# Kernel optimization log

Measured on AMD Instinct MI355X. Metric: run time of the kernel, lower is better.

The kernel has to match this reference:

```python
import jax, jax.numpy as jnp
import numpy as np

B, N, K = 4, 20480, 16
LAMDA = 2.0  # config.lfa_param

def _gather(pc, idx):
    # pc: [B, N, D], idx: [B, N, K] -> [B, N, K, D]
    return jax.vmap(lambda p, i: p[i])(pc, idx)

def _cbr(x, W, g, b, act=True):
    # 1x1 conv (no bias) + BN(eval, affine) + optional ReLU; x: [B, C, N, K]
    y = jnp.einsum('oc,bcnk->bonk', W, x)
    y = y * g[None, :, None, None] + b[None, :, None, None]
    return jnp.maximum(y, 0.0) if act else y

def _fdis(feat, f_nb):
    # feat: [B, C, N], f_nb: [B, C, N, K] -> exp(-mean_c |diff|): [B, 1, N, K]
    return jnp.exp(-jnp.mean(jnp.abs(feat[..., None] - f_nb), axis=1, keepdims=True))

def _pool(f_set, f_dis, g_dis, fcW, mW, mg, mb):
    # Dualdis_Att_Pool: softmax attention over neighbor dim K
    concat = jnp.concatenate([g_dis, f_dis * LAMDA, f_set], axis=1)
    att = jax.nn.softmax(jnp.einsum('oc,bcnk->bonk', fcW, concat), axis=3)
    f_lc = jnp.sum(f_set * att, axis=-1, keepdims=True)
    return _cbr(f_lc, mW, mg, mb)

def _forward(feature, xyz, m1_W, m1_g, m1_b, lm1_W, lm1_g, lm1_b, lm2_W, lm2_g, lm2_b, p1fc_W, p1m_W, p1m_g, p1m_b, p2fc_W, p2m_W, p2m_g, p2m_b, m2_W, m2_g, m2_b, sc_W, sc_g, sc_b, m3_W, m3_g, m3_b, m4_W, m4_g, m4_b, neigh_idx):
    f_pc = _cbr(feature, m1_W, m1_g, m1_b)               # [B,16,N,1]
    # --- local polar representation ---
    nb = _gather(xyz, neigh_idx)                         # [B,N,K,3]
    xyz_t = xyz[:, :, None, :]
    rel = xyz_t - nb
    r_alpha = jnp.arctan2(rel[..., 1], rel[..., 0])[..., None]
    r_beta = jnp.arctan2(rel[..., 2], jnp.sqrt(rel[..., 0]**2 + rel[..., 1]**2))[..., None]
    r_dis = jnp.sqrt(jnp.sum(rel * rel, axis=-1, keepdims=True))
    rel_info = jnp.concatenate([r_dis, jnp.broadcast_to(xyz_t, nb.shape), nb], axis=-1)
    g_dis = jnp.exp(-r_dis)                              # [B,N,K,1]
    local_vol = jnp.max(r_dis[..., 0], axis=-1) ** 3     # [B,N]
    dirv = xyz - jnp.mean(nb, axis=2)                    # [B,N,3]
    d_alpha = jnp.arctan2(dirv[..., 1], dirv[..., 0])[:, :, None, None]
    d_beta = jnp.arctan2(dirv[..., 2], jnp.sqrt(dirv[..., 0]**2 + dirv[..., 1]**2))[:, :, None, None]
    angle = jnp.concatenate([r_alpha - d_alpha, r_beta - d_beta], axis=-1)
    local_rep = jnp.concatenate([angle, rel_info], axis=-1)  # [B,N,K,9]
    g_vol = jnp.sqrt(jnp.sum(xyz * xyz, axis=-1)) ** 3
    lg_ratio = (local_vol / g_vol)[..., None]            # [B,N,1]
    g_dis = jnp.transpose(g_dis, (0, 3, 1, 2))           # [B,1,N,K]
    lrep = _cbr(jnp.transpose(local_rep, (0, 3, 1, 2)), lm1_W, lm1_g, lm1_b)  # [B,16,N,K]
    # --- dual-distance attentive pooling 1 ---
    feat0 = f_pc[..., 0]
    f_nb = jnp.transpose(_gather(jnp.transpose(feat0, (0, 2, 1)), neigh_idx), (0, 3, 1, 2))
    f_cat = jnp.concatenate([f_nb, lrep], axis=1)        # [B,32,N,K]
    f_lc = _pool(f_cat, _fdis(feat0, f_nb), g_dis, p1fc_W, p1m_W, p1m_g, p1m_b)  # [B,16,N,1]
    # --- dual-distance attentive pooling 2 ---
    lrep2 = _cbr(lrep, lm2_W, lm2_g, lm2_b)
    feat1 = f_lc[..., 0]
    f_nb2 = jnp.transpose(_gather(jnp.transpose(feat1, (0, 2, 1)), neigh_idx), (0, 3, 1, 2))
    f_cat2 = jnp.concatenate([f_nb2, lrep2], axis=1)     # [B,32,N,K]
    f_lc2 = _pool(f_cat2, _fdis(feat1, f_nb2), g_dis, p2fc_W, p2m_W, p2m_g, p2m_b)  # [B,32,N,1]
    # --- residual head ---
    out_lc = _cbr(f_lc2, m2_W, m2_g, m2_b, act=False)
    sc = _cbr(feature, sc_W, sc_g, sc_b, act=False)
    f_gc_in = jnp.transpose(jnp.concatenate([xyz, lg_ratio], axis=-1), (0, 2, 1))[..., None]
    f_gc = _cbr(f_gc_in, m3_W, m3_g, m3_b, act=False)
    return _cbr(jnp.concatenate([out_lc + sc, f_gc], axis=1), m4_W, m4_g, m4_b)  # [B,64,N,1]

def setup_inputs():
    key = jax.random.key(0)
    ks = iter(jax.random.split(key, 48))
    def rn(shape, s=1.0):
        return jax.random.normal(next(ks), shape, jnp.float32) * s
    inp = {"feature": rn((B, 16, N, 1)), "xyz": rn((B, N, 3))}
    def wgb(name, co, ci):
        inp[name + "_W"] = rn((co, ci), 0.1)
        inp[name + "_g"] = jax.random.uniform(next(ks), (co,), jnp.float32, 0.5, 1.5)
        inp[name + "_b"] = jnp.zeros((co,), jnp.float32)
    wgb("m1", 16, 16); wgb("lm1", 16, 9); wgb("lm2", 16, 16)
    inp["p1fc_W"] = rn((32, 34), 0.1); wgb("p1m", 16, 32)
    inp["p2fc_W"] = rn((32, 34), 0.1); wgb("p2m", 32, 32)
    wgb("m2", 64, 32); wgb("sc", 64, 16); wgb("m3", 64, 4); wgb("m4", 64, 128)
    inp["neigh_idx"] = jax.random.randint(next(ks), (B, N, K), 0, N)
    return inp

def reference(feature, xyz, m1_W, m1_g, m1_b, lm1_W, lm1_g, lm1_b, lm2_W, lm2_g, lm2_b, p1fc_W, p1m_W, p1m_g, p1m_b, p2fc_W, p2m_W, p2m_g, p2m_b, m2_W, m2_g, m2_b, sc_W, sc_g, sc_b, m3_W, m3_g, m3_b, m4_W, m4_g, m4_b, neigh_idx):
    return _forward(feature, xyz, m1_W, m1_g, m1_b, lm1_W, lm1_g, lm1_b, lm2_W, lm2_g, lm2_b, p1fc_W, p1m_W, p1m_g, p1m_b, p2fc_W, p2m_W, p2m_g, p2m_b, m2_W, m2_g, m2_b, sc_W, sc_g, sc_b, m3_W, m3_g, m3_b, m4_W, m4_g, m4_b, neigh_idx)
```

## Files before the change

kernel.cpp:

```cpp
#include <hip/hip_runtime.h>

#define NN 20480
#define NPTS 81920
#define MS 36
#define RSH 40
#define PTSH 640
#define MIDOFF 2560
#define LOG2E 1.4426950408889634f

#define P1MWT 0
#define P2MWT 512
#define MAWT  1536
#define MXWT  3584
#define MVWT  4608
#define C0WT  4864
#define BFB   4928
#define WTOT  6976

#define WL_P2M 0
#define WL_MA  1024
#define WL_MX  3072
#define WL_MV  4096
#define WL_C0  4352
#define WOFF   4416
#define SLAB   1280
#define LGRO   (WOFF + 4*SLAB)
#define SMTOT2 9600

typedef _Float16 half8 __attribute__((ext_vector_type(8)));
typedef float f32x4 __attribute__((ext_vector_type(4)));

__device__ __forceinline__ float redsum16(float v){
    v += __shfl_xor(v, 1); v += __shfl_xor(v, 2);
    v += __shfl_xor(v, 4); v += __shfl_xor(v, 8);
    return v;
}
__device__ __forceinline__ float redmax16(float v){
    v = fmaxf(v, __shfl_xor(v, 1)); v = fmaxf(v, __shfl_xor(v, 2));
    v = fmaxf(v, __shfl_xor(v, 4)); v = fmaxf(v, __shfl_xor(v, 8));
    return v;
}
__device__ __forceinline__ void wsync(){
    __builtin_amdgcn_wave_barrier();
    __threadfence_block();
    __builtin_amdgcn_wave_barrier();
}
__device__ __forceinline__ float frcp(float x){ return __builtin_amdgcn_rcpf(x); }

__device__ __forceinline__ unsigned int ph(float lo, float hi){
    union { _Float16 h[2]; unsigned int u; } cv;
    cv.h[0] = (_Float16)lo; cv.h[1] = (_Float16)hi;
    return cv.u;
}
__device__ __forceinline__ float2 unph(unsigned int u){
    union { unsigned int u; _Float16 h[2]; } cv; cv.u = u;
    return make_float2((float)cv.h[0], (float)cv.h[1]);
}
__device__ __forceinline__ float h2f(short s){
    union { short s; _Float16 h; } cv; cv.s = s;
    return (float)cv.h;
}

__device__ __forceinline__ float fatan2(float y, float x){
    float ax = fabsf(x), ay = fabsf(y);
    float mx = fmaxf(ax, ay), mn = fminf(ax, ay);
    float z = mn * frcp(mx);
    z = (mx == 0.f) ? 0.f : z;
    float z2 = z * z;
    float a = fmaf(0.05265332f, z2, -0.11643287f);
    a = fmaf(a, z2, 0.19354346f);
    a = fmaf(a, z2, -0.33262347f);
    a = fmaf(a, z2, 0.99997726f);
    a = a * z;
    a = (ay > ax) ? (1.5707963268f - a) : a;
    a = (x < 0.f) ? (3.1415926536f - a) : a;
    return (y < 0.f) ? -a : a;
}

__device__ __forceinline__ int swiz(int bid){
    int x = bid & 7, s = bid >> 3;
    return ((x >> 1) * 2560) + ((x & 1) * 1280) + s;
}
__device__ __forceinline__ int swizC(int bid){
    int x = bid & 7, s = bid >> 3;
    return x * 160 + s;
}

__global__ void k_fill4(float4* out, float val, int n4){
    int i = blockIdx.x * blockDim.x + threadIdx.x;
    int stride = gridDim.x * blockDim.x;
    float4 v = make_float4(val, val, val, val);
    for (; i < n4; i += stride) out[i] = v;
}

__global__ void k_prep(
    const float* __restrict__ p1fc, const float* __restrict__ p2fc,
    const float* __restrict__ p1mW, const float* __restrict__ p2mW,
    const float* __restrict__ m2W,  const float* __restrict__ scW,
    const float* __restrict__ m3W,  const float* __restrict__ m4W,
    const float* __restrict__ m2g,  const float* __restrict__ m2b,
    const float* __restrict__ scg,  const float* __restrict__ scb,
    const float* __restrict__ m3g,  const float* __restrict__ m3b,
    float* __restrict__ wb)
{
    int bid = blockIdx.x;
    if (bid == 0){
        for (int e = threadIdx.x; e < 512; e += 256)
            wb[P1MWT + e] = p1mW[e];
    } else if (bid == 1){
        for (int e = threadIdx.x; e < 1024; e += 256){
            int c = e >> 5, r = e & 31;
            int k = r >> 1, h = r & 1;
            wb[P2MWT + e] = p2mW[(k + 16*h)*32 + c];
        }
    } else if (bid == 2){
        for (int e = threadIdx.x; e < 2048; e += 256){
            int c = e >> 6, r = e & 63;
            int o = (r >> 2) + 16*(r & 3);
            float acc = 0.f;
            for (int h = 0; h < 64; h++)
                acc = fmaf(m4W[o*128 + h] * m2g[h], m2W[h*32 + c], acc);
            wb[MAWT + e] = acc;
        }
    } else if (bid == 3){
        for (int e = threadIdx.x; e < 1024; e += 256){
            int c = e >> 6, r = e & 63;
            int o = (r >> 2) + 16*(r & 3);
            float acc = 0.f;
            for (int h = 0; h < 64; h++)
                acc = fmaf(m4W[o*128 + h] * scg[h], scW[h*16 + c], acc);
            wb[MXWT + e] = acc;
        }
    } else if (bid == 4){
        int e = threadIdx.x;
        if (e < 256){
            int c = e >> 6, r = e & 63;
            int o = (r >> 2) + 16*(r & 3);
            float acc = 0.f;
            for (int h = 0; h < 64; h++)
                acc = fmaf(m4W[o*128 + 64 + h] * m3g[h], m3W[h*4 + c], acc);
            wb[MVWT + e] = acc;
        }
        if (e < 64){
            int o = (e >> 2) + 16*(e & 3);
            float acc = 0.f;
            for (int h = 0; h < 64; h++){
                acc = fmaf(m4W[o*128 + h], m2b[h] + scb[h], acc);
                acc = fmaf(m4W[o*128 + 64 + h], m3b[h], acc);
            }
            wb[C0WT + e] = acc;
        }
    } else if (bid == 6 || bid == 7){
        const float* src = (bid == 6) ? p1fc : p2fc;
        short* dst = (short*)(wb + BFB) + (bid - 6) * 2048;
        for (int e = threadIdx.x; e < 2048; e += 256){
            int j = e & 7, l = (e >> 3) & 63, tq = (e >> 9) & 3;
            int q = tq & 1, t = tq >> 1;
            int kk = ((l >> 4) << 3) + j;
            int c = q*32 + kk;
            int o = (l & 15) + 16*t;
            float v = (c < 34) ? src[o*34 + c] * LOG2E : 0.f;
            union { _Float16 h; short s; } cv; cv.h = (_Float16)v;
            dst[e] = cv.s;
        }
    }
}

__global__ __launch_bounds__(256) void k_feat0(
    const float* __restrict__ featp,
    const float* __restrict__ m1W,
    const float* __restrict__ m1g,
    const float* __restrict__ m1b,
    float* __restrict__ feat0)
{
    int p = blockIdx.x * 256 + threadIdx.x;
    if (p >= NPTS) return;
    int b = p / NN;
    int n = p - b * NN;
    float x[16];
    #pragma unroll
    for (int c = 0; c < 16; c++) x[c] = featp[(b*16 + c)*NN + n];
    float o[16];
    for (int oo = 0; oo < 16; oo++){
        float acc = 0.f;
        #pragma unroll
        for (int c = 0; c < 16; c++) acc = fmaf(m1W[oo*16 + c], x[c], acc);
        o[oo] = fmaxf(fmaf(m1g[oo], acc, m1b[oo]), 0.f);
    }
    float4* dst = (float4*)(feat0 + (size_t)p * 16);
    #pragma unroll
    for (int i = 0; i < 4; i++)
        dst[i] = make_float4(o[4*i], o[4*i+1], o[4*i+2], o[4*i+3]);
}

__device__ __forceinline__ float poolT(f32x4 a, const short* base, int c, int g){
    const short* xc = base + c;
    float x0 = h2f(xc[(g*4 + 0)*RSH]), x1 = h2f(xc[(g*4 + 1)*RSH]);
    float x2 = h2f(xc[(g*4 + 2)*RSH]), x3 = h2f(xc[(g*4 + 3)*RSH]);
    float m = fmaxf(fmaxf(a[0], a[1]), fmaxf(a[2], a[3]));
    m = fmaxf(m, __shfl_xor(m, 16)); m = fmaxf(m, __shfl_xor(m, 32));
    float e0 = exp2f(a[0] - m), e1 = exp2f(a[1] - m);
    float e2 = exp2f(a[2] - m), e3 = exp2f(a[3] - m);
    float s = (e0 + e1) + (e2 + e3);
    float num = fmaf(e3, x3, fmaf(e2, x2, fmaf(e1, x1, e0*x0)));
    s   += __shfl_xor(s, 16);   s   += __shfl_xor(s, 32);
    num += __shfl_xor(num, 16); num += __shfl_xor(num, 32);
    return num * frcp(s);
}

__device__ __forceinline__ void phaseB_mfma(
    const short* xs, const short* bfS, float* smMid, int tid)
{
    const half8* bf = (const half8*)bfS;
    const int l = tid & 63, wv = tid >> 6;
    const int o = l & 15, g = l >> 4;
    half8 B00 = bf[l], B01 = bf[64 + l], B10 = bf[128 + l], B11 = bf[192 + l];
    #pragma unroll 2
    for (int pp = 0; pp < 4; pp++){
        const int pt = wv*4 + pp;
        const short* base = xs + pt*PTSH;
        const short* rowp = base + (l & 15)*RSH;
        half8 A0 = *(const half8*)(rowp + g*8);
        unsigned int d = *(const unsigned int*)(rowp + 32);
        union { unsigned int u[4]; half8 v; } a1u;
        a1u.u[0] = (g == 0) ? d : 0u;
        a1u.u[1] = 0u; a1u.u[2] = 0u; a1u.u[3] = 0u;
        half8 A1 = a1u.v;
        f32x4 z = {0.f, 0.f, 0.f, 0.f};
        f32x4 a0 = __builtin_amdgcn_mfma_f32_16x16x32_f16(A0, B00, z, 0, 0, 0);
        a0       = __builtin_amdgcn_mfma_f32_16x16x32_f16(A1, B01, a0, 0, 0, 0);
        f32x4 a1 = __builtin_amdgcn_mfma_f32_16x16x32_f16(A0, B10, z, 0, 0, 0);
        a1       = __builtin_amdgcn_mfma_f32_16x16x32_f16(A1, B11, a1, 0, 0, 0);
        float mid0 = poolT(a0, base, 2 + o,      g);
        float mid1 = poolT(a1, base, 2 + o + 16, g);
        if (g == 0){
            smMid[pt*MS + o]      = mid0;
            smMid[pt*MS + o + 16] = mid1;
        }
    }
}

__global__ __launch_bounds__(128, 2) void k_stage1(
    const float* __restrict__ xyzp,
    const int* __restrict__ nidx,
    const float* __restrict__ feat0,
    const float* __restrict__ lm1W,
    const float* __restrict__ lm1g,
    const float* __restrict__ lm1b,
    const float* __restrict__ wb,
    const float* __restrict__ p1mg,
    const float* __restrict__ p1mb,
    float* __restrict__ feat1)
{
    __shared__ float sm[2848];
    short* xs = (short*)sm;
    const int k  = threadIdx.x & 15;
    const int pt = threadIdx.x >> 4;
    const int p  = (swiz(blockIdx.x) << 3) + pt;
    const int b  = p / NN;

    {
        const int ii = nidx[(p << 4) + k];
        const int q  = b * NN + ii;
        const float4* an = (const float4*)(feat0 + (size_t)q * 16);
        const float4* as = (const float4*)(feat0 + (size_t)p * 16);
        const float sx = xyzp[p*3 + 0];
        const float sy = xyzp[p*3 + 1];
        const float sz = xyzp[p*3 + 2];
        const float nx = xyzp[q*3 + 0];
        const float ny = xyzp[q*3 + 1];
        const float nz = xyzp[q*3 + 2];

        float4 A0 = an[0], A1 = an[1], A2 = an[2], A3 = an[3];
        float sd = 0.f;
        {
            float4 S0 = as[0], S1 = as[1], S2 = as[2], S3 = as[3];
            sd += fabsf(S0.x-A0.x) + fabsf(S0.y-A0.y) + fabsf(S0.z-A0.z) + fabsf(S0.w-A0.w);
            sd += fabsf(S1.x-A1.x) + fabsf(S1.y-A1.y) + fabsf(S1.z-A1.z) + fabsf(S1.w-A1.w);
            sd += fabsf(S2.x-A2.x) + fabsf(S2.y-A2.y) + fabsf(S2.z-A2.z) + fabsf(S2.w-A2.w);
            sd += fabsf(S3.x-A3.x) + fabsf(S3.y-A3.y) + fabsf(S3.z-A3.z) + fabsf(S3.w-A3.w);
        }
        float fdis2 = 2.f * __expf(-sd * 0.0625f);

        float rx = sx - nx, ry = sy - ny, rz = sz - nz;
        float r2 = rx*rx + ry*ry;
        float rdis = sqrtf(r2 + rz*rz);
        float ralpha = fatan2(ry, rx);
        float rbeta  = fatan2(rz, sqrtf(r2));
        float gdis = __expf(-rdis);

        float mx = redsum16(nx) * 0.0625f;
        float my = redsum16(ny) * 0.0625f;
        float mz = redsum16(nz) * 0.0625f;
        float dx = sx - mx, dy = sy - my, dz = sz - mz;
        float dalpha = fatan2(dy, dx);
        float dbeta  = fatan2(dz, sqrtf(dx*dx + dy*dy));

        float rep[9] = { ralpha - dalpha, rbeta - dbeta, rdis, sx, sy, sz, nx, ny, nz };
        float lrep[16];
        #pragma unroll
        for (int o = 0; o < 16; o++){
            float acc = 0.f;
            #pragma unroll
            for (int c = 0; c < 9; c++) acc = fmaf(lm1W[o*9 + c], rep[c], acc);
            lrep[o] = fmaxf(fmaf(lm1g[o], acc, lm1b[o]), 0.f);
        }

        uint4* rp = (uint4*)(xs + pt*PTSH + k*RSH);
        uint4 U;
        U.x = ph(gdis, fdis2); U.y = ph(A0.x, A0.y);
        U.z = ph(A0.z, A0.w);  U.w = ph(A1.x, A1.y);
        rp[0] = U;
        U.x = ph(A1.z, A1.w);  U.y = ph(A2.x, A2.y);
        U.z = ph(A2.z, A2.w);  U.w = ph(A3.x, A3.y);
        rp[1] = U;
        U.x = ph(A3.z, A3.w);      U.y = ph(lrep[0], lrep[1]);
        U.z = ph(lrep[2], lrep[3]); U.w = ph(lrep[4], lrep[5]);
        rp[2] = U;
        U.x = ph(lrep[6], lrep[7]);   U.y = ph(lrep[8], lrep[9]);
        U.z = ph(lrep[10], lrep[11]); U.w = ph(lrep[12], lrep[13]);
        rp[3] = U;
        U.x = ph(lrep[14], lrep[15]); U.y = 0u; U.z = 0u; U.w = 0u;
        rp[4] = U;
    }
    wsync();

    phaseB_mfma(xs, (const short*)(wb + BFB), sm + MIDOFF, threadIdx.x);
    wsync();

    {
        float mid[32];
        const float4* mp = (const float4*)(sm + MIDOFF + pt*MS);
        #pragma unroll
        for (int i = 0; i < 8; i++){
            float4 t = mp[i];
            mid[4*i]=t.x; mid[4*i+1]=t.y; mid[4*i+2]=t.z; mid[4*i+3]=t.w;
        }
        const float4* wp = (const float4*)(wb + P1MWT) + (k << 3);
        float acc = 0.f;
        #pragma unroll
        for (int i = 0; i < 8; i++){
            float4 wv = wp[i];
            acc = fmaf(wv.x, mid[4*i],   acc);
            acc = fmaf(wv.y, mid[4*i+1], acc);
            acc = fmaf(wv.z, mid[4*i+2], acc);
            acc = fmaf(wv.w, mid[4*i+3], acc);
        }
        feat1[(size_t)(p << 4) + k] = fmaxf(fmaf(p1mg[k], acc, p1mb[k]), 0.f);
    }
}

__global__ __launch_bounds__(128, 2) void k_s2ab(
    const float* __restrict__ xyzp,
    const int* __restrict__ nidx,
    const float* __restrict__ feat1,
    const float* __restrict__ lm1W,
    const float* __restrict__ lm1g,
    const float* __restrict__ lm1b,
    const float* __restrict__ lm2W,
    const float* __restrict__ lm2g,
    const float* __restrict__ lm2b,
    const float* __restrict__ wb,
    float* __restrict__ outp)
{
    __shared__ float sm[2848];
    short* xs = (short*)sm;
    const int k    = threadIdx.x & 15;
    const int pt   = threadIdx.x >> 4;
    const int pblk = swiz(blockIdx.x);
    const int p    = (pblk << 3) + pt;
    const int b    = p / NN;
    const int n    = p - b * NN;
    float lgrv;

    {
        const int ii = nidx[(p << 4) + k];
        const int q  = b * NN + ii;
        const float4* an = (const float4*)(feat1 + (size_t)q * 16);
        const float4* as = (const float4*)(feat1 + (size_t)p * 16);
        const float sx = xyzp[p*3 + 0];
        const float sy = xyzp[p*3 + 1];
        const float sz = xyzp[p*3 + 2];
        const float nx = xyzp[q*3 + 0];
        const float ny = xyzp[q*3 + 1];
        const float nz = xyzp[q*3 + 2];

        float4 A0 = an[0], A1 = an[1], A2 = an[2], A3 = an[3];
        float sd = 0.f;
        {
            float4 S0 = as[0], S1 = as[1], S2 = as[2], S3 = as[3];
            sd += fabsf(S0.x-A0.x) + fabsf(S0.y-A0.y) + fabsf(S0.z-A0.z) + fabsf(S0.w-A0.w);
            sd += fabsf(S1.x-A1.x) + fabsf(S1.y-A1.y) + fabsf(S1.z-A1.z) + fabsf(S1.w-A1.w);
            sd += fabsf(S2.x-A2.x) + fabsf(S2.y-A2.y) + fabsf(S2.z-A2.z) + fabsf(S2.w-A2.w);
            sd += fabsf(S3.x-A3.x) + fabsf(S3.y-A3.y) + fabsf(S3.z-A3.z) + fabsf(S3.w-A3.w);
        }
        float fdis2 = 2.f * __expf(-sd * 0.0625f);

        float rx = sx - nx, ry = sy - ny, rz = sz - nz;
        float r2 = rx*rx + ry*ry;
        float rdis = sqrtf(r2 + rz*rz);
        float ralpha = fatan2(ry, rx);
        float rbeta  = fatan2(rz, sqrtf(r2));
        float gdis = __expf(-rdis);

        float mx = redsum16(nx) * 0.0625f;
        float my = redsum16(ny) * 0.0625f;
        float mz = redsum16(nz) * 0.0625f;
        float dx = sx - mx, dy = sy - my, dz = sz - mz;
        float dalpha = fatan2(dy, dx);
        float dbeta  = fatan2(dz, sqrtf(dx*dx + dy*dy));

        float mxd = redmax16(rdis);
        float nr  = sqrtf(sx*sx + sy*sy + sz*sz);
        lgrv = (mxd*mxd*mxd) * frcp(nr*nr*nr);

        float rep[9] = { ralpha - dalpha, rbeta - dbeta, rdis, sx, sy, sz, nx, ny, nz };
        float lrep[16];
        #pragma unroll
        for (int o = 0; o < 16; o++){
            float acc = 0.f;
            #pragma unroll
            for (int c = 0; c < 9; c++) acc = fmaf(lm1W[o*9 + c], rep[c], acc);
            lrep[o] = fmaxf(fmaf(lm1g[o], acc, lm1b[o]), 0.f);
        }
        float lrep2[16];
        #pragma unroll
        for (int o = 0; o < 16; o++){
            float acc = 0.f;
            #pragma unroll
            for (int c = 0; c < 16; c++) acc = fmaf(lm2W[o*16 + c], lrep[c], acc);
            lrep2[o] = fmaxf(fmaf(lm2g[o], acc, lm2b[o]), 0.f);
        }

        uint4* rp = (uint4*)(xs + pt*PTSH + k*RSH);
        uint4 U;
        U.x = ph(gdis, fdis2); U.y = ph(A0.x, A0.y);
        U.z = ph(A0.z, A0.w);  U.w = ph(A1.x, A1.y);
        rp[0] = U;
        U.x = ph(A1.z, A1.w);  U.y = ph(A2.x, A2.y);
        U.z = ph(A2.z, A2.w);  U.w = ph(A3.x, A3.y);
        rp[1] = U;
        U.x = ph(A3.z, A3.w);        U.y = ph(lrep2[0], lrep2[1]);
        U.z = ph(lrep2[2], lrep2[3]); U.w = ph(lrep2[4], lrep2[5]);
        rp[2] = U;
        U.x = ph(lrep2[6], lrep2[7]);   U.y = ph(lrep2[8], lrep2[9]);
        U.z = ph(lrep2[10], lrep2[11]); U.w = ph(lrep2[12], lrep2[13]);
        rp[3] = U;
        U.x = ph(lrep2[14], lrep2[15]); U.y = 0u; U.z = 0u; U.w = 0u;
        rp[4] = U;
    }
    wsync();

    phaseB_mfma(xs, (const short*)(wb + BFB) + 2048, sm + MIDOFF, threadIdx.x);
    wsync();

    {
        float m0 = sm[MIDOFF + pt*MS + 2*k];
        float m1 = sm[MIDOFF + pt*MS + 2*k + 1];
        unsigned int u = ph(m0, m1);
        ((unsigned int*)outp)[(size_t)(b*64 + k)*NN + n] = u;
        if (k == 0) outp[(size_t)(b*64 + 16)*NN + n] = lgrv;
    }
}

__global__ __launch_bounds__(256, 2) void k_s2c(
    const float* __restrict__ featp,
    const float* __restrict__ xyzp,
    const float* __restrict__ wb,
    const float* __restrict__ p2mg,
    const float* __restrict__ p2mb,
    const float* __restrict__ m4g,
    const float* __restrict__ m4b,
    float* __restrict__ outp)
{
    __shared__ float sm[SMTOT2];
    const int tid = threadIdx.x;
    const int k   = tid & 15;
    const int g   = (tid >> 4) & 3;
    const int w   = tid >> 6;
    const int pblk = swizC(blockIdx.x);
    const int p0  = pblk << 6;
    const int b   = p0 / NN;
    const int n0  = p0 - b * NN;
    const int ptg = g*4;
    const int nT  = n0 + w*16 + ptg;
    float* slab = sm + WOFF + w*SLAB;

    for (int e = tid; e < 4416; e += 256) sm[e] = wb[512 + e];
    {
        uint4 um = *(const uint4*)((const unsigned int*)outp +
                                   (size_t)(b*64 + k)*NN + nT);
        float2 f;
        f = unph(um.x);
        slab[(ptg+0)*36 + 2*k] = f.x; slab[(ptg+0)*36 + 2*k+1] = f.y;
        f = unph(um.y);
        slab[(ptg+1)*36 + 2*k] = f.x; slab[(ptg+1)*36 + 2*k+1] = f.y;
        f = unph(um.z);
        slab[(ptg+2)*36 + 2*k] = f.x; slab[(ptg+2)*36 + 2*k+1] = f.y;
        f = unph(um.w);
        slab[(ptg+3)*36 + 2*k] = f.x; slab[(ptg+3)*36 + 2*k+1] = f.y;
        if (k == 0){
            float4 lv = *(const float4*)(outp + (size_t)(b*64 + 16)*NN + nT);
            sm[LGRO + w*16 + ptg + 0] = lv.x; sm[LGRO + w*16 + ptg + 1] = lv.y;
            sm[LGRO + w*16 + ptg + 2] = lv.z; sm[LGRO + w*16 + ptg + 3] = lv.w;
        }
    }
    __syncthreads();

    {
        const float2* wp = (const float2*)(sm + WL_P2M);
        float aA[4] = {0.f,0.f,0.f,0.f}, aB[4] = {0.f,0.f,0.f,0.f};
        #pragma unroll 2
        for (int cq = 0; cq < 8; cq++){
            f32x4 mv[4];
            #pragma unroll
            for (int i = 0; i < 4; i++)
                mv[i] = *(const f32x4*)(slab + (ptg+i)*36 + cq*4);
            #pragma unroll
            for (int cc = 0; cc < 4; cc++){
                float2 wv = wp[(cq*4+cc)*16 + k];
                #pragma unroll
                for (int i = 0; i < 4; i++){
                    aA[i] = fmaf(wv.x, mv[i][cc], aA[i]);
                    aB[i] = fmaf(wv.y, mv[i][cc], aB[i]);
                }
            }
        }
        float gA = p2mg[k], bA = p2mb[k], gB = p2mg[k+16], bB = p2mb[k+16];
        #pragma unroll
        for (int i = 0; i < 4; i++){
            slab[576 + (ptg+i)*36 + k]      = fmaxf(fmaf(gA, aA[i], bA), 0.f);
            slab[576 + (ptg+i)*36 + k + 16] = fmaxf(fmaf(gB, aB[i], bB), 0.f);
        }
    }
    wsync();

    float o4[4][4];
    {
        f32x4 c0v = *(const f32x4*)(sm + WL_C0 + 4*k);
        #pragma unroll
        for (int j = 0; j < 4; j++)
            #pragma unroll
            for (int i = 0; i < 4; i++) o4[j][i] = c0v[j];

        const f32x4* wa = (const f32x4*)(sm + WL_MA);
        #pragma unroll 2
        for (int cq = 0; cq < 8; cq++){
            f32x4 av[4];
            #pragma unroll
            for (int i = 0; i < 4; i++)
                av[i] = *(const f32x4*)(slab + 576 + (ptg+i)*36 + cq*4);
            #pragma unroll
            for (int cc = 0; cc < 4; cc++){
                f32x4 wv = wa[(cq*4+cc)*16 + k];
                #pragma unroll
                for (int i = 0; i < 4; i++){
                    #pragma unroll
                    for (int j = 0; j < 4; j++)
                        o4[j][i] = fmaf(wv[j], av[i][cc], o4[j][i]);
                }
            }
        }
        const f32x4* wx = (const f32x4*)(sm + WL_MX);
        #pragma unroll 4
        for (int c = 0; c < 16; c++){
            f32x4 wv = wx[c*16 + k];
            f32x4 xv = *(const f32x4*)(featp + (size_t)(b*16 + c)*NN + nT);
            #pragma unroll
            for (int i = 0; i < 4; i++){
                #pragma unroll
                for (int j = 0; j < 4; j++)
                    o4[j][i] = fmaf(wv[j], xv[i], o4[j][i]);
            }
        }
        const f32x4* wvv = (const f32x4*)(sm + WL_MV);
        #pragma unroll
        for (int c = 0; c < 3; c++){
            f32x4 wv = wvv[c*16 + k];
            #pragma unroll
            for (int i = 0; i < 4; i++){
                float vc = xyzp[(size_t)(p0 + w*16 + ptg + i)*3 + c];
                #pragma unroll
                for (int j = 0; j < 4; j++)
                    o4[j][i] = fmaf(wv[j], vc, o4[j][i]);
            }
        }
        {
            f32x4 wv = wvv[3*16 + k];
            #pragma unroll
            for (int i = 0; i < 4; i++){
                float vc = sm[LGRO + w*16 + ptg + i];
                #pragma unroll
                for (int j = 0; j < 4; j++)
                    o4[j][i] = fmaf(wv[j], vc, o4[j][i]);
            }
        }
    }
    wsync();

    {
        float* stg = slab;
        #pragma unroll
        for (int j = 0; j < 4; j++){
            int oo = k + 16*j;
            float gv = m4g[oo], bv = m4b[oo];
            #pragma unroll
            for (int i = 0; i < 4; i++)
                stg[oo*20 + ptg + i] = fmaxf(fmaf(gv, o4[j][i], bv), 0.f);
        }
        wsync();
        const int l = tid & 63;
        float* dst = outp + (size_t)(b*64 + l)*NN + n0 + w*16;
        #pragma unroll
        for (int q = 0; q < 4; q++){
            f32x4 v = *(const f32x4*)(stg + l*20 + q*4);
            *(f32x4*)(dst + q*4) = v;
        }
    }
}

extern "C" void kernel_launch(void* const* d_in, const int* in_sizes, int n_in,
                              void* d_out, int out_size, void* d_ws, size_t ws_size,
                              hipStream_t stream) {
    float* outp = (float*)d_out;

    float fillv = 1.0f;
    bool ok = true;
    if (n_in != 32) { fillv = 5.0f; ok = false; }
    else if (in_sizes[0] != 1310720 || in_sizes[1] != 245760 ||
             in_sizes[31] != 1310720) { fillv = 7.0f; ok = false; }
    else if (out_size != 5242880) { fillv = 9.0f; ok = false; }
    else if (ws_size < ((size_t)NPTS * 16 + WTOT) * sizeof(float)) { fillv = 11.0f; ok = false; }

    if (!ok){
        k_fill4<<<1024, 256, 0, stream>>>((float4*)outp, fillv, out_size/4);
        return;
    }

    const float* featp = (const float*)d_in[0];
    const float* xyzp  = (const float*)d_in[1];
    const int*   nidx  = (const int*)d_in[31];

    float* feat0 = (float*)d_out;
    float* feat1 = (float*)d_ws;
    float* wb    = (float*)d_ws + (size_t)NPTS * 16;

    #define W(i) ((const float*)d_in[2 + (i)])
    k_prep<<<8, 256, 0, stream>>>(W(9), W(13), W(10), W(14), W(17), W(20),
                                  W(23), W(26),
                                  W(18), W(19), W(21), W(22), W(24), W(25),
                                  wb);
    k_feat0<<<NPTS/256, 256, 0, stream>>>(featp, W(0), W(1), W(2), feat0);
    k_stage1<<<NPTS/8, 128, 0, stream>>>(xyzp, nidx, feat0,
        W(3), W(4), W(5), wb, W(11), W(12), feat1);
    k_s2ab<<<NPTS/8, 128, 0, stream>>>(xyzp, nidx, feat1,
        W(3), W(4), W(5),
        W(6), W(7), W(8),
        wb, outp);
    k_s2c<<<NPTS/64, 256, 0, stream>>>(featp, xyzp, wb,
        W(15), W(16),
        W(27), W(28),
        outp);
    #undef W
}
```

Before: 253.7 us.

## Store intermediates in fp16, split lm1 linearly, reuse geometry across stages

Merges weight prep and the m1 conv into one launch, stores feat0/feat1 as fp16, and splits the lm1 conv into per-point center and neighbor partial sums precomputed once. Stage 1 writes the angles, distance and volume ratio to scratch rows of the output, so stage 2 reads them instead of redoing the gathers, atan2 and reductions. L1 feature distances are computed with packed half arithmetic. This cuts gather bandwidth and redundant math, at the cost of extra fp16 rounding error and more scratch traffic.

```diff
diff --git a/kernel.cpp b/kernel.cpp
--- a/kernel.cpp
+++ b/kernel.cpp
@@ -6,7 +6,13 @@
 #define RSH 40
 #define PTSH 640
 #define MIDOFF 2560
+#define HSOFF 2848
 #define LOG2E 1.4426950408889634f
+
+#define HSROW 17
+#define PAROW 25
+#define PBROW 41
+#define LGROW 57
 
 #define P1MWT 0
 #define P2MWT 512
@@ -15,20 +21,13 @@
 #define MVWT  4608
 #define C0WT  4864
 #define BFB   4928
-#define WTOT  6976
-
-#define WL_P2M 0
-#define WL_MA  1024
-#define WL_MX  3072
-#define WL_MV  4096
-#define WL_C0  4352
-#define WOFF   4416
-#define SLAB   1280
-#define LGRO   (WOFF + 4*SLAB)
-#define SMTOT2 9600
+#define LM1AW 6976
+#define WTOT  7040
 
 typedef _Float16 half8 __attribute__((ext_vector_type(8)));
+typedef _Float16 h2t  __attribute__((ext_vector_type(2)));
 typedef float f32x4 __attribute__((ext_vector_type(4)));
+union HU { unsigned int u; h2t h; };
 
 __device__ __forceinline__ float redsum16(float v){
     v += __shfl_xor(v, 1); v += __shfl_xor(v, 2);
@@ -56,9 +55,15 @@
     union { unsigned int u; _Float16 h[2]; } cv; cv.u = u;
     return make_float2((float)cv.h[0], (float)cv.h[1]);
 }
-__device__ __forceinline__ float h2f(short s){
-    union { short s; _Float16 h; } cv; cv.s = s;
-    return (float)cv.h;
+
+__device__ __forceinline__ float sd16(uint4 a0, uint4 a1, uint4 b0, uint4 b1){
+    HU acc; acc.u = 0u;
+    #define SDT(A,B) { HU x,y,d; x.u=(A); y.u=(B); d.h = x.h - y.h; \
+                       d.u &= 0x7FFF7FFFu; acc.h = acc.h + d.h; }
+    SDT(a0.x,b0.x) SDT(a0.y,b0.y) SDT(a0.z,b0.z) SDT(a0.w,b0.w)
+    SDT(a1.x,b1.x) SDT(a1.y,b1.y) SDT(a1.z,b1.z) SDT(a1.w,b1.w)
+    #undef SDT
+    return (float)acc.h[0] + (float)acc.h[1];
 }
 
 __device__ __forceinline__ float fatan2(float y, float x){
@@ -93,7 +98,12 @@
     for (; i < n4; i += stride) out[i] = v;
 }
 
-__global__ void k_prep(
+__global__ __launch_bounds__(256) void k_pre(
+    const float* __restrict__ featp, const float* __restrict__ xyzp,
+    const float* __restrict__ m1W,  const float* __restrict__ m1g,
+    const float* __restrict__ m1b,
+    const float* __restrict__ lm1W, const float* __restrict__ lm1g,
+    const float* __restrict__ lm1b,
     const float* __restrict__ p1fc, const float* __restrict__ p2fc,
     const float* __restrict__ p1mW, const float* __restrict__ p2mW,
     const float* __restrict__ m2W,  const float* __restrict__ scW,
@@ -101,102 +111,126 @@
     const float* __restrict__ m2g,  const float* __restrict__ m2b,
     const float* __restrict__ scg,  const float* __restrict__ scb,
     const float* __restrict__ m3g,  const float* __restrict__ m3b,
-    float* __restrict__ wb)
+    float* __restrict__ wb, float* __restrict__ wsF,
+    float* __restrict__ outp)
 {
     int bid = blockIdx.x;
-    if (bid == 0){
-        for (int e = threadIdx.x; e < 512; e += 256)
-            wb[P1MWT + e] = p1mW[e];
-    } else if (bid == 1){
-        for (int e = threadIdx.x; e < 1024; e += 256){
-            int c = e >> 5, r = e & 31;
-            int k = r >> 1, h = r & 1;
-            wb[P2MWT + e] = p2mW[(k + 16*h)*32 + c];
-        }
-    } else if (bid == 2){
-        for (int e = threadIdx.x; e < 2048; e += 256){
-            int c = e >> 6, r = e & 63;
-            int o = (r >> 2) + 16*(r & 3);
-            float acc = 0.f;
-            for (int h = 0; h < 64; h++)
-                acc = fmaf(m4W[o*128 + h] * m2g[h], m2W[h*32 + c], acc);
-            wb[MAWT + e] = acc;
-        }
-    } else if (bid == 3){
-        for (int e = threadIdx.x; e < 1024; e += 256){
-            int c = e >> 6, r = e & 63;
-            int o = (r >> 2) + 16*(r & 3);
-            float acc = 0.f;
-            for (int h = 0; h < 64; h++)
-                acc = fmaf(m4W[o*128 + h] * scg[h], scW[h*16 + c], acc);
-            wb[MXWT + e] = acc;
-        }
-    } else if (bid == 4){
-        int e = threadIdx.x;
-        if (e < 256){
-            int c = e >> 6, r = e & 63;
-            int o = (r >> 2) + 16*(r & 3);
-            float acc = 0.f;
-            for (int h = 0; h < 64; h++)
-                acc = fmaf(m4W[o*128 + 64 + h] * m3g[h], m3W[h*4 + c], acc);
-            wb[MVWT + e] = acc;
-        }
-        if (e < 64){
-            int o = (e >> 2) + 16*(e & 3);
-            float acc = 0.f;
-            for (int h = 0; h < 64; h++){
-                acc = fmaf(m4W[o*128 + h], m2b[h] + scb[h], acc);
-                acc = fmaf(m4W[o*128 + 64 + h], m3b[h], acc);
-            }
-            wb[C0WT + e] = acc;
-        }
-    } else if (bid == 6 || bid == 7){
-        const float* src = (bid == 6) ? p1fc : p2fc;
-        short* dst = (short*)(wb + BFB) + (bid - 6) * 2048;
-        for (int e = threadIdx.x; e < 2048; e += 256){
-            int j = e & 7, l = (e >> 3) & 63, tq = (e >> 9) & 3;
-            int q = tq & 1, t = tq >> 1;
-            int kk = ((l >> 4) << 3) + j;
-            int c = q*32 + kk;
-            int o = (l & 15) + 16*t;
-            float v = (c < 34) ? src[o*34 + c] * LOG2E : 0.f;
-            union { _Float16 h; short s; } cv; cv.h = (_Float16)v;
-            dst[e] = cv.s;
-        }
-    }
-}
-
-__global__ __launch_bounds__(256) void k_feat0(
-    const float* __restrict__ featp,
-    const float* __restrict__ m1W,
-    const float* __restrict__ m1g,
-    const float* __restrict__ m1b,
-    float* __restrict__ feat0)
-{
-    int p = blockIdx.x * 256 + threadIdx.x;
-    if (p >= NPTS) return;
+    if (bid < 8){
+        if (bid == 0){
+            for (int e = threadIdx.x; e < 512; e += 256)
+                wb[P1MWT + e] = p1mW[e];
+        } else if (bid == 1){
+            for (int e = threadIdx.x; e < 1024; e += 256){
+                int c = e >> 5, r = e & 31;
+                int k = r >> 1, h = r & 1;
+                wb[P2MWT + e] = p2mW[(k + 16*h)*32 + c];
+            }
+        } else if (bid == 2){
+            for (int e = threadIdx.x; e < 2048; e += 256){
+                int c = e >> 6, r = e & 63;
+                int o = (r >> 2) + 16*(r & 3);
+                float acc = 0.f;
+                for (int h = 0; h < 64; h++)
+                    acc = fmaf(m4W[o*128 + h] * m2g[h], m2W[h*32 + c], acc);
+                wb[MAWT + e] = acc;
+            }
+        } else if (bid == 3){
+            for (int e = threadIdx.x; e < 1024; e += 256){
+                int c = e >> 6, r = e & 63;
+                int o = (r >> 2) + 16*(r & 3);
+                float acc = 0.f;
+                for (int h = 0; h < 64; h++)
+                    acc = fmaf(m4W[o*128 + h] * scg[h], scW[h*16 + c], acc);
+                wb[MXWT + e] = acc;
+            }
+        } else if (bid == 4){
+            int e = threadIdx.x;
+            if (e < 256){
+                int c = e >> 6, r = e & 63;
+                int o = (r >> 2) + 16*(r & 3);
+                float acc = 0.f;
+                for (int h = 0; h < 64; h++)
+                    acc = fmaf(m4W[o*128 + 64 + h] * m3g[h], m3W[h*4 + c], acc);
+                wb[MVWT + e] = acc;
+            }
+            if (e < 64){
+                int o = (e >> 2) + 16*(e & 3);
+                float acc = 0.f;
+                for (int h = 0; h < 64; h++){
+                    acc = fmaf(m4W[o*128 + h], m2b[h] + scb[h], acc);
+                    acc = fmaf(m4W[o*128 + 64 + h], m3b[h], acc);
+                }
+                wb[C0WT + e] = acc;
+            }
+        } else if (bid == 5){
+            int e = threadIdx.x;
+            if (e < 48){
+                int c = e >> 4, o = e & 15;
+                wb[LM1AW + e] = lm1g[o] * lm1W[o*9 + c];
+            }
+        } else {
+            const float* src = (bid == 6) ? p1fc : p2fc;
+            short* dst = (short*)(wb + BFB) + (bid - 6) * 2048;
+            for (int e = threadIdx.x; e < 2048; e += 256){
+                int j = e & 7, l = (e >> 3) & 63, tq = (e >> 9) & 3;
+                int q = tq & 1, t = tq >> 1;
+                int kk = ((l >> 4) << 3) + j;
+                int c = q*32 + kk;
+                int o = (l & 15) + 16*t;
+                float v = (c < 34) ? src[o*34 + c] * LOG2E : 0.f;
+                union { _Float16 h; short s; } cv; cv.h = (_Float16)v;
+                dst[e] = cv.s;
+            }
+        }
+        return;
+    }
+    int p = (bid - 8) * 256 + threadIdx.x;
     int b = p / NN;
     int n = p - b * NN;
     float x[16];
     #pragma unroll
     for (int c = 0; c < 16; c++) x[c] = featp[(b*16 + c)*NN + n];
-    float o[16];
-    for (int oo = 0; oo < 16; oo++){
-        float acc = 0.f;
-        #pragma unroll
-        for (int c = 0; c < 16; c++) acc = fmaf(m1W[oo*16 + c], x[c], acc);
-        o[oo] = fmaxf(fmaf(m1g[oo], acc, m1b[oo]), 0.f);
-    }
-    float4* dst = (float4*)(feat0 + (size_t)p * 16);
-    #pragma unroll
-    for (int i = 0; i < 4; i++)
-        dst[i] = make_float4(o[4*i], o[4*i+1], o[4*i+2], o[4*i+3]);
+    unsigned int dw[8];
+    for (int oo = 0; oo < 8; oo++){
+        float v0 = 0.f, v1 = 0.f;
+        #pragma unroll
+        for (int c = 0; c < 16; c++){
+            v0 = fmaf(m1W[(2*oo)*16 + c],   x[c], v0);
+            v1 = fmaf(m1W[(2*oo+1)*16 + c], x[c], v1);
+        }
+        v0 = fmaxf(fmaf(m1g[2*oo],   v0, m1b[2*oo]),   0.f);
+        v1 = fmaxf(fmaf(m1g[2*oo+1], v1, m1b[2*oo+1]), 0.f);
+        dw[oo] = ph(v0, v1);
+    }
+    uint4* f0 = (uint4*)(outp + (size_t)b*64*NN + (size_t)n*8);
+    f0[0] = make_uint4(dw[0], dw[1], dw[2], dw[3]);
+    f0[1] = make_uint4(dw[4], dw[5], dw[6], dw[7]);
+
+    float sx = xyzp[p*3 + 0], sy = xyzp[p*3 + 1], sz = xyzp[p*3 + 2];
+    unsigned int* outu = (unsigned int*)outp;
+    unsigned short* hnT = (unsigned short*)wsF + (size_t)NPTS*16;
+    unsigned int hw[8];
+    for (int d = 0; d < 8; d++){
+        float h0, h1, g0, g1;
+        int o0 = 2*d, o1 = 2*d+1;
+        h0 = lm1g[o0]*(lm1W[o0*9+3]*sx + lm1W[o0*9+4]*sy + lm1W[o0*9+5]*sz) + lm1b[o0];
+        h1 = lm1g[o1]*(lm1W[o1*9+3]*sx + lm1W[o1*9+4]*sy + lm1W[o1*9+5]*sz) + lm1b[o1];
+        g0 = lm1g[o0]*(lm1W[o0*9+6]*sx + lm1W[o0*9+7]*sy + lm1W[o0*9+8]*sz);
+        g1 = lm1g[o1]*(lm1W[o1*9+6]*sx + lm1W[o1*9+7]*sy + lm1W[o1*9+8]*sz);
+        outu[((size_t)b*64 + HSROW + d)*NN + n] = ph(h0, h1);
+        hw[d] = ph(g0, g1);
+    }
+    uint4* hq = (uint4*)(hnT + (size_t)p*16);
+    hq[0] = make_uint4(hw[0], hw[1], hw[2], hw[3]);
+    hq[1] = make_uint4(hw[4], hw[5], hw[6], hw[7]);
 }
 
 __device__ __forceinline__ float poolT(f32x4 a, const short* base, int c, int g){
     const short* xc = base + c;
-    float x0 = h2f(xc[(g*4 + 0)*RSH]), x1 = h2f(xc[(g*4 + 1)*RSH]);
-    float x2 = h2f(xc[(g*4 + 2)*RSH]), x3 = h2f(xc[(g*4 + 3)*RSH]);
+    union { short s; _Float16 h; } c0, c1, c2, c3;
+    c0.s = xc[(g*4 + 0)*RSH]; c1.s = xc[(g*4 + 1)*RSH];
+    c2.s = xc[(g*4 + 2)*RSH]; c3.s = xc[(g*4 + 3)*RSH];
+    float x0 = (float)c0.h, x1 = (float)c1.h, x2 = (float)c2.h, x3 = (float)c3.h;
     float m = fmaxf(fmaxf(a[0], a[1]), fmaxf(a[2], a[3]));
     m = fmaxf(m, __shfl_xor(m, 16)); m = fmaxf(m, __shfl_xor(m, 32));
     float e0 = exp2f(a[0] - m), e1 = exp2f(a[1] - m);
@@ -240,30 +274,61 @@
     }
 }
 
+__device__ __forceinline__ void lrep16(
+    const float* __restrict__ la, float da, float db, float rd,
+    const float* hsS, uint4 H0, uint4 H1, unsigned int* lw)
+{
+    unsigned int hn[8] = {H0.x, H0.y, H0.z, H0.w, H1.x, H1.y, H1.z, H1.w};
+    #pragma unroll
+    for (int d = 0; d < 8; d++){
+        HU a, b, s;
+        a.u = __float_as_uint(hsS[d]);
+        b.u = hn[d];
+        s.h = a.h + b.h;
+        int o0 = 2*d, o1 = 2*d+1;
+        float v0 = fmaf(la[o0], da, fmaf(la[16+o0], db, la[32+o0]*rd));
+        float v1 = fmaf(la[o1], da, fmaf(la[16+o1], db, la[32+o1]*rd));
+        v0 = fmaxf(v0 + (float)s.h[0], 0.f);
+        v1 = fmaxf(v1 + (float)s.h[1], 0.f);
+        lw[d] = ph(v0, v1);
+    }
+}
+
 __global__ __launch_bounds__(128, 2) void k_stage1(
     const float* __restrict__ xyzp,
     const int* __restrict__ nidx,
-    const float* __restrict__ feat0,
-    const float* __restrict__ lm1W,
-    const float* __restrict__ lm1g,
-    const float* __restrict__ lm1b,
     const float* __restrict__ wb,
     const float* __restrict__ p1mg,
     const float* __restrict__ p1mb,
-    float* __restrict__ feat1)
+    float* __restrict__ wsF,
+    float* __restrict__ outp)
 {
-    __shared__ float sm[2848];
+    __shared__ float sm[2912];
     short* xs = (short*)sm;
     const int k  = threadIdx.x & 15;
     const int pt = threadIdx.x >> 4;
-    const int p  = (swiz(blockIdx.x) << 3) + pt;
+    const int lane = threadIdx.x & 63, wv = threadIdx.x >> 6;
+    const int pblk = swiz(blockIdx.x);
+    const int p  = (pblk << 3) + pt;
     const int b  = p / NN;
+    const int n  = p - b * NN;
+    const int nb = (pblk << 3) - b * NN;
+    unsigned short* hnT = (unsigned short*)wsF + (size_t)NPTS*16;
+
+    if (lane < 32){
+        int lpt = wv*4 + (lane >> 3), d = lane & 7;
+        sm[HSOFF + wv*32 + lane] =
+            outp[((size_t)b*64 + HSROW + d)*NN + nb + lpt];
+    }
+    wsync();
 
     {
         const int ii = nidx[(p << 4) + k];
         const int q  = b * NN + ii;
-        const float4* an = (const float4*)(feat0 + (size_t)q * 16);
-        const float4* as = (const float4*)(feat0 + (size_t)p * 16);
+        const uint4* aq = (const uint4*)(outp + (size_t)b*64*NN + (size_t)ii*8);
+        const uint4* ap = (const uint4*)(outp + (size_t)b*64*NN + (size_t)n*8);
+        uint4 A0 = aq[0], A1 = aq[1];
+        uint4 S0 = ap[0], S1 = ap[1];
         const float sx = xyzp[p*3 + 0];
         const float sy = xyzp[p*3 + 1];
         const float sz = xyzp[p*3 + 2];
@@ -271,15 +336,7 @@
         const float ny = xyzp[q*3 + 1];
         const float nz = xyzp[q*3 + 2];
 
-        float4 A0 = an[0], A1 = an[1], A2 = an[2], A3 = an[3];
-        float sd = 0.f;
-        {
-            float4 S0 = as[0], S1 = as[1], S2 = as[2], S3 = as[3];
-            sd += fabsf(S0.x-A0.x) + fabsf(S0.y-A0.y) + fabsf(S0.z-A0.z) + fabsf(S0.w-A0.w);
-            sd += fabsf(S1.x-A1.x) + fabsf(S1.y-A1.y) + fabsf(S1.z-A1.z) + fabsf(S1.w-A1.w);
-            sd += fabsf(S2.x-A2.x) + fabsf(S2.y-A2.y) + fabsf(S2.z-A2.z) + fabsf(S2.w-A2.w);
-            sd += fabsf(S3.x-A3.x) + fabsf(S3.y-A3.y) + fabsf(S3.z-A3.z) + fabsf(S3.w-A3.w);
-        }
+        float sd = sd16(A0, A1, S0, S1);
         float fdis2 = 2.f * __expf(-sd * 0.0625f);
 
         float rx = sx - nx, ry = sy - ny, rz = sz - nz;
@@ -295,33 +352,29 @@
         float dx = sx - mx, dy = sy - my, dz = sz - mz;
         float dalpha = fatan2(dy, dx);
         float dbeta  = fatan2(dz, sqrtf(dx*dx + dy*dy));
-
-        float rep[9] = { ralpha - dalpha, rbeta - dbeta, rdis, sx, sy, sz, nx, ny, nz };
-        float lrep[16];
-        #pragma unroll
-        for (int o = 0; o < 16; o++){
-            float acc = 0.f;
-            #pragma unroll
-            for (int c = 0; c < 9; c++) acc = fmaf(lm1W[o*9 + c], rep[c], acc);
-            lrep[o] = fmaxf(fmaf(lm1g[o], acc, lm1b[o]), 0.f);
-        }
+        float da = ralpha - dalpha, db = rbeta - dbeta;
+
+        float mxd = redmax16(rdis);
+        float nr  = sqrtf(sx*sx + sy*sy + sz*sz);
+
+        unsigned int* outu = (unsigned int*)outp;
+        outu[((size_t)b*64 + PAROW + k)*NN + n] = ph(da, db);
+        outu[((size_t)b*64 + PBROW + k)*NN + n] = ph(rdis, gdis);
+        if (k == 0)
+            outp[((size_t)b*64 + LGROW)*NN + n] = (mxd*mxd*mxd) * frcp(nr*nr*nr);
+
+        const uint4* hq = (const uint4*)(hnT + (size_t)q*16);
+        uint4 H0 = hq[0], H1 = hq[1];
+        unsigned int lw[8];
+        lrep16(wb + LM1AW, da, db, rdis,
+               sm + HSOFF + wv*32 + (pt & 3)*8, H0, H1, lw);
 
         uint4* rp = (uint4*)(xs + pt*PTSH + k*RSH);
-        uint4 U;
-        U.x = ph(gdis, fdis2); U.y = ph(A0.x, A0.y);
-        U.z = ph(A0.z, A0.w);  U.w = ph(A1.x, A1.y);
-        rp[0] = U;
-        U.x = ph(A1.z, A1.w);  U.y = ph(A2.x, A2.y);
-        U.z = ph(A2.z, A2.w);  U.w = ph(A3.x, A3.y);
-        rp[1] = U;
-        U.x = ph(A3.z, A3.w);      U.y = ph(lrep[0], lrep[1]);
-        U.z = ph(lrep[2], lrep[3]); U.w = ph(lrep[4], lrep[5]);
-        rp[2] = U;
-        U.x = ph(lrep[6], lrep[7]);   U.y = ph(lrep[8], lrep[9]);
-        U.z = ph(lrep[10], lrep[11]); U.w = ph(lrep[12], lrep[13]);
-        rp[3] = U;
-        U.x = ph(lrep[14], lrep[15]); U.y = 0u; U.z = 0u; U.w = 0u;
-        rp[4] = U;
+        rp[0] = make_uint4(ph(gdis, fdis2), A0.x, A0.y, A0.z);
+        rp[1] = make_uint4(A0.w, A1.x, A1.y, A1.z);
+        rp[2] = make_uint4(A1.w, lw[0], lw[1], lw[2]);
+        rp[3] = make_uint4(lw[3], lw[4], lw[5], lw[6]);
+        rp[4] = make_uint4(lw[7], 0u, 0u, 0u);
     }
     wsync();
 
@@ -340,114 +393,96 @@
         float acc = 0.f;
         #pragma unroll
         for (int i = 0; i < 8; i++){
-            float4 wv = wp[i];
-            acc = fmaf(wv.x, mid[4*i],   acc);
-            acc = fmaf(wv.y, mid[4*i+1], acc);
-            acc = fmaf(wv.z, mid[4*i+2], acc);
-            acc = fmaf(wv.w, mid[4*i+3], acc);
-        }
-        feat1[(size_t)(p << 4) + k] = fmaxf(fmaf(p1mg[k], acc, p1mb[k]), 0.f);
+            float4 wv4 = wp[i];
+            acc = fmaf(wv4.x, mid[4*i],   acc);
+            acc = fmaf(wv4.y, mid[4*i+1], acc);
+            acc = fmaf(wv4.z, mid[4*i+2], acc);
+            acc = fmaf(wv4.w, mid[4*i+3], acc);
+        }
+        float v = fmaxf(fmaf(p1mg[k], acc, p1mb[k]), 0.f);
+        union { _Float16 h; unsigned short s; } cv; cv.h = (_Float16)v;
+        ((unsigned short*)wsF)[(size_t)(p << 4) + k] = cv.s;
     }
 }
 
 __global__ __launch_bounds__(128, 2) void k_s2ab(
-    const float* __restrict__ xyzp,
     const int* __restrict__ nidx,
-    const float* __restrict__ feat1,
-    const float* __restrict__ lm1W,
-    const float* __restrict__ lm1g,
-    const float* __restrict__ lm1b,
     const float* __restrict__ lm2W,
     const float* __restrict__ lm2g,
     const float* __restrict__ lm2b,
     const float* __restrict__ wb,
+    const float* __restrict__ wsF,
     float* __restrict__ outp)
 {
-    __shared__ float sm[2848];
+    __shared__ float sm[2912];
     short* xs = (short*)sm;
     const int k    = threadIdx.x & 15;
     const int pt   = threadIdx.x >> 4;
+    const int lane = threadIdx.x & 63, wv = threadIdx.x >> 6;
     const int pblk = swiz(blockIdx.x);
     const int p    = (pblk << 3) + pt;
     const int b    = p / NN;
     const int n    = p - b * NN;
-    float lgrv;
+    const int nb   = (pblk << 3) - b * NN;
+    const unsigned short* feat1h = (const unsigned short*)wsF;
+    const unsigned short* hnT = (const unsigned short*)wsF + (size_t)NPTS*16;
+
+    if (lane < 32){
+        int lpt = wv*4 + (lane >> 3), d = lane & 7;
+        sm[HSOFF + wv*32 + lane] =
+            outp[((size_t)b*64 + HSROW + d)*NN + nb + lpt];
+    }
+    wsync();
 
     {
         const int ii = nidx[(p << 4) + k];
         const int q  = b * NN + ii;
-        const float4* an = (const float4*)(feat1 + (size_t)q * 16);
-        const float4* as = (const float4*)(feat1 + (size_t)p * 16);
-        const float sx = xyzp[p*3 + 0];
-        const float sy = xyzp[p*3 + 1];
-        const float sz = xyzp[p*3 + 2];
-        const float nx = xyzp[q*3 + 0];
-        const float ny = xyzp[q*3 + 1];
-        const float nz = xyzp[q*3 + 2];
-
-        float4 A0 = an[0], A1 = an[1], A2 = an[2], A3 = an[3];
-        float sd = 0.f;
-        {
-            float4 S0 = as[0], S1 = as[1], S2 = as[2], S3 = as[3];
-            sd += fabsf(S0.x-A0.x) + fabsf(S0.y-A0.y) + fabsf(S0.z-A0.z) + fabsf(S0.w-A0.w);
-            sd += fabsf(S1.x-A1.x) + fabsf(S1.y-A1.y) + fabsf(S1.z-A1.z) + fabsf(S1.w-A1.w);
-            sd += fabsf(S2.x-A2.x) + fabsf(S2.y-A2.y) + fabsf(S2.z-A2.z) + fabsf(S2.w-A2.w);
-            sd += fabsf(S3.x-A3.x) + fabsf(S3.y-A3.y) + fabsf(S3.z-A3.z) + fabsf(S3.w-A3.w);
-        }
+        const unsigned int* outu = (const unsigned int*)outp;
+        unsigned int pa = outu[((size_t)b*64 + PAROW + k)*NN + n];
+        unsigned int pb = outu[((size_t)b*64 + PBROW + k)*NN + n];
+        float2 dab = unph(pa);
+        HU pbu; pbu.u = pb;
+        float rd = (float)pbu.h[0];
+
+        const uint4* aq = (const uint4*)(feat1h + (size_t)q*16);
+        const uint4* ap = (const uint4*)(feat1h + (size_t)p*16);
+        uint4 A0 = aq[0], A1 = aq[1];
+        uint4 S0 = ap[0], S1 = ap[1];
+        float sd = sd16(A0, A1, S0, S1);
         float fdis2 = 2.f * __expf(-sd * 0.0625f);
 
-        float rx = sx - nx, ry = sy - ny, rz = sz - nz;
-        float r2 = rx*rx + ry*ry;
-        float rdis = sqrtf(r2 + rz*rz);
-        float ralpha = fatan2(ry, rx);
-        float rbeta  = fatan2(rz, sqrtf(r2));
-        float gdis = __expf(-rdis);
-
-        float mx = redsum16(nx) * 0.0625f;
-        float my = redsum16(ny) * 0.0625f;
-        float mz = redsum16(nz) * 0.0625f;
-        float dx = sx - mx, dy = sy - my, dz = sz - mz;
-        float dalpha = fatan2(dy, dx);
-        float dbeta  = fatan2(dz, sqrtf(dx*dx + dy*dy));
-
-        float mxd = redmax16(rdis);
-        float nr  = sqrtf(sx*sx + sy*sy + sz*sz);
-        lgrv = (mxd*mxd*mxd) * frcp(nr*nr*nr);
-
-        float rep[9] = { ralpha - dalpha, rbeta - dbeta, rdis, sx, sy, sz, nx, ny, nz };
-        float lrep[16];
-        #pragma unroll
-        for (int o = 0; o < 16; o++){
-            float acc = 0.f;
-            #pragma unroll
-            for (int c = 0; c < 9; c++) acc = fmaf(lm1W[o*9 + c], rep[c], acc);
-            lrep[o] = fmaxf(fmaf(lm1g[o], acc, lm1b[o]), 0.f);
-        }
-        float lrep2[16];
-        #pragma unroll
-        for (int o = 0; o < 16; o++){
-            float acc = 0.f;
-            #pragma unroll
-            for (int c = 0; c < 16; c++) acc = fmaf(lm2W[o*16 + c], lrep[c], acc);
-            lrep2[o] = fmaxf(fmaf(lm2g[o], acc, lm2b[o]), 0.f);
-        }
-
+        const uint4* hq = (const uint4*)(hnT + (size_t)q*16);
+        uint4 H0 = hq[0], H1 = hq[1];
+        unsigned int lw[8];
+        lrep16(wb + LM1AW, dab.x, dab.y, rd,
+               sm + HSOFF + wv*32 + (pt & 3)*8, H0, H1, lw);
+
+        float lr[16];
+        #pragma unroll
+        for (int d = 0; d < 8; d++){
+            float2 f = unph(lw[d]);
+            lr[2*d] = f.x; lr[2*d+1] = f.y;
+        }
+        unsigned int l2[8];
+        for (int oo = 0; oo < 8; oo++){
+            float v0 = 0.f, v1 = 0.f;
+            #pragma unroll
+            for (int c = 0; c < 16; c++){
+                v0 = fmaf(lm2W[(2*oo)*16 + c],   lr[c], v0);
+                v1 = fmaf(lm2W[(2*oo+1)*16 + c], lr[c], v1);
+            }
+            v0 = fmaxf(fmaf(lm2g[2*oo],   v0, lm2b[2*oo]),   0.f);
+            v1 = fmaxf(fmaf(lm2g[2*oo+1], v1, lm2b[2*oo+1]), 0.f);
+            l2[oo] = ph(v0, v1);
+        }
+
+        HU g0; g0.h[0] = pbu.h[1]; g0.h[1] = (_Float16)fdis2;
         uint4* rp = (uint4*)(xs + pt*PTSH + k*RSH);
-        uint4 U;
-        U.x = ph(gdis, fdis2); U.y = ph(A0.x, A0.y);
-        U.z = ph(A0.z, A0.w);  U.w = ph(A1.x, A1.y);
-        rp[0] = U;
-        U.x = ph(A1.z, A1.w);  U.y = ph(A2.x, A2.y);
-        U.z = ph(A2.z, A2.w);  U.w = ph(A3.x, A3.y);
-        rp[1] = U;
-        U.x = ph(A3.z, A3.w);        U.y = ph(lrep2[0], lrep2[1]);
-        U.z = ph(lrep2[2], lrep2[3]); U.w = ph(lrep2[4], lrep2[5]);
-        rp[2] = U;
-        U.x = ph(lrep2[6], lrep2[7]);   U.y = ph(lrep2[8], lrep2[9]);
-        U.z = ph(lrep2[10], lrep2[11]); U.w = ph(lrep2[12], lrep2[13]);
-        rp[3] = U;
-        U.x = ph(lrep2[14], lrep2[15]); U.y = 0u; U.z = 0u; U.w = 0u;
-        rp[4] = U;
+        rp[0] = make_uint4(g0.u, A0.x, A0.y, A0.z);
+        rp[1] = make_uint4(A0.w, A1.x, A1.y, A1.z);
+        rp[2] = make_uint4(A1.w, l2[0], l2[1], l2[2]);
+        rp[3] = make_uint4(l2[3], l2[4], l2[5], l2[6]);
+        rp[4] = make_uint4(l2[7], 0u, 0u, 0u);
     }
     wsync();
 
@@ -457,11 +492,19 @@
     {
         float m0 = sm[MIDOFF + pt*MS + 2*k];
         float m1 = sm[MIDOFF + pt*MS + 2*k + 1];
-        unsigned int u = ph(m0, m1);
-        ((unsigned int*)outp)[(size_t)(b*64 + k)*NN + n] = u;
-        if (k == 0) outp[(size_t)(b*64 + 16)*NN + n] = lgrv;
-    }
-}
+        ((unsigned int*)outp)[(size_t)(b*64 + k)*NN + n] = ph(m0, m1);
+    }
+}
+
+#define WL_P2M 0
+#define WL_MA  1024
+#define WL_MX  3072
+#define WL_MV  4096
+#define WL_C0  4352
+#define WOFF   4416
+#define SLAB   1280
+#define LGRO   (WOFF + 4*SLAB)
+#define SMTOT2 9600
 
 __global__ __launch_bounds__(256, 2) void k_s2c(
     const float* __restrict__ featp,
@@ -500,7 +543,7 @@
         f = unph(um.w);
         slab[(ptg+3)*36 + 2*k] = f.x; slab[(ptg+3)*36 + 2*k+1] = f.y;
         if (k == 0){
-            float4 lv = *(const float4*)(outp + (size_t)(b*64 + 16)*NN + nT);
+            float4 lv = *(const float4*)(outp + (size_t)(b*64 + LGROW)*NN + nT);
             sm[LGRO + w*16 + ptg + 0] = lv.x; sm[LGRO + w*16 + ptg + 1] = lv.y;
             sm[LGRO + w*16 + ptg + 2] = lv.z; sm[LGRO + w*16 + ptg + 3] = lv.w;
         }
@@ -641,22 +684,25 @@
     const float* xyzp  = (const float*)d_in[1];
     const int*   nidx  = (const int*)d_in[31];
 
-    float* feat0 = (float*)d_out;
-    float* feat1 = (float*)d_ws;
-    float* wb    = (float*)d_ws + (size_t)NPTS * 16;
+    float* wsF = (float*)d_ws;
+    float* wb  = (float*)d_ws + (size_t)NPTS * 16;
 
     #define W(i) ((const float*)d_in[2 + (i)])
-    k_prep<<<8, 256, 0, stream>>>(W(9), W(13), W(10), W(14), W(17), W(20),
-                                  W(23), W(26),
-                                  W(18), W(19), W(21), W(22), W(24), W(25),
-                                  wb);
-    k_feat0<<<NPTS/256, 256, 0, stream>>>(featp, W(0), W(1), W(2), feat0);
-    k_stage1<<<NPTS/8, 128, 0, stream>>>(xyzp, nidx, feat0,
-        W(3), W(4), W(5), wb, W(11), W(12), feat1);
-    k_s2ab<<<NPTS/8, 128, 0, stream>>>(xyzp, nidx, feat1,
+    k_pre<<<8 + NPTS/256, 256, 0, stream>>>(
+        featp, xyzp,
+        W(0), W(1), W(2),
         W(3), W(4), W(5),
+        W(9), W(13),
+        W(10), W(14),
+        W(17), W(20), W(23), W(26),
+        W(18), W(19), W(21), W(22), W(24), W(25),
+        wb, wsF, outp);
+    k_stage1<<<NPTS/8, 128, 0, stream>>>(xyzp, nidx, wb,
+        W(11), W(12),
+        wsF, outp);
+    k_s2ab<<<NPTS/8, 128, 0, stream>>>(nidx,
         W(6), W(7), W(8),
-        wb, outp);
+        wb, wsF, outp);
     k_s2c<<<NPTS/64, 256, 0, stream>>>(featp, xyzp, wb,
         W(15), W(16),
         W(27), W(28),
```

Result: no change. 252.6 us (-0.4%).
